# Performance work log

Hardware: AMD Instinct MI355X
Metric: run time of the kernel (lower is better)

## Reference

```python
import jax, jax.numpy as jnp
import numpy as np

EMB = 1024
CTX = 32
F_IN, R, F_OUT = 1024, 16, 1024
N_EXP = 16
H1 = 2048   # expert / gating hidden
H2 = 512    # expert output width
B = 8


def _init(key, shape, fan_in):
    return jax.random.normal(key, shape, dtype=jnp.float32) / np.sqrt(fan_in)


def setup_inputs() -> dict:
    key = jax.random.key(0)
    ks = jax.random.split(key, 14)
    return {
        "s": jax.random.normal(ks[0], (B, EMB), dtype=jnp.float32),
        # gating: Linear(EMB,2048) -> ReLU -> Linear(2048,N_EXP) -> Softmax
        "Wg1": _init(ks[1], (EMB, H1), EMB),
        "bg1": jnp.zeros((H1,), jnp.float32),
        "Wg2": _init(ks[2], (H1, N_EXP), H1),
        "bg2": jnp.zeros((N_EXP,), jnp.float32),
        # experts (stacked): Linear(EMB+CTX,2048) -> ReLU -> Linear(2048,512)
        "W1": _init(ks[3], (N_EXP, EMB + CTX, H1), EMB + CTX),
        "b1": jnp.zeros((N_EXP, H1), jnp.float32),
        "W2": _init(ks[4], (N_EXP, H1, H2), H1),
        "b2": jnp.zeros((N_EXP, H2), jnp.float32),
        # decoders
        "WA": _init(ks[5], (H2, F_IN * R), H2),
        "bA": jnp.zeros((F_IN * R,), jnp.float32),
        "WB": _init(ks[6], (H2, R * F_OUT), H2),
        "bB": jnp.zeros((R * F_OUT,), jnp.float32),
    }


def reference(s, Wg1, bg1, Wg2, bg2, W1, b1, W2, b2, WA, bA, WB, bB):
    # gating weights over experts: [B, E]
    weights = jax.nn.softmax(jax.nn.relu(s @ Wg1 + bg1) @ Wg2 + bg2, axis=-1)

    # Expert layer-1. Input is concat([s, one_hot(c)]); since the context part
    # is a one-hot, its contribution is just a row of the context block of W1.
    W1s = W1[:, :EMB, :]              # [E, EMB, H1]
    W1c = W1[:, EMB:, :]              # [E, CTX, H1]
    base = jnp.einsum('bi,eih->ebh', s, W1s) + b1[:, None, :]   # [E, B, H1]
    # h[c,e,b,:] = relu(base[e,b,:] + W1c[e,c,:])
    h = jax.nn.relu(base[None] + jnp.transpose(W1c, (1, 0, 2))[:, :, None, :])  # [C,E,B,H1]

    # Expert layer-2: [C, E, B, H2]
    eo = jnp.einsum('cebh,ehd->cebd', h, W2) + b2[None, :, None, :]

    # softmax-weighted mixture over experts: [C, B, H2]
    z = jnp.einsum('be,cebd->cbd', weights, eo)

    A = (z @ WA + bA).reshape(CTX, B, F_IN, R)
    Bm = (z @ WB + bB).reshape(CTX, B, R, F_OUT)
    return A, Bm
```

## Files before the change

### kernel.cpp

```cpp
#include <hip/hip_runtime.h>
#include <hip/hip_bf16.h>

#define EMB 1024
#define CTX 32
#define NEXP 16
#define H1 2048
#define H2 512
#define NBIG 16384

typedef __attribute__((ext_vector_type(8))) short short8;
typedef __attribute__((ext_vector_type(4))) float floatx4;
typedef __attribute__((ext_vector_type(2))) unsigned uint2v;
typedef const __attribute__((address_space(1))) void* gas_t;
typedef __attribute__((address_space(3))) void* las_t;

__device__ __forceinline__ void gl16(const unsigned short* g, unsigned short* l) {
  __builtin_amdgcn_global_load_lds((gas_t)(const void*)g, (las_t)(void*)l, 16, 0, 0);
}

__device__ inline unsigned short bf_bits(float x) {
  unsigned u = __builtin_bit_cast(unsigned, x);
  u += 0x7fffu + ((u >> 16) & 1u);
  return (unsigned short)(u >> 16);
}
__device__ inline unsigned pk_bf16(float a, float b) {
  return (unsigned)bf_bits(a) | ((unsigned)bf_bits(b) << 16);
}

__global__ void __launch_bounds__(512) k_fusedA(const float* __restrict__ s,
                                                const float* __restrict__ Wg1,
                                                const float* __restrict__ bg1,
                                                const float* __restrict__ W1,
                                                const float* __restrict__ b1,
                                                const float* __restrict__ W2,
                                                float* __restrict__ g1,
                                                float* __restrict__ base,
                                                unsigned short* __restrict__ W2t) {
  __shared__ __align__(16) char smem[34816];
  int bid = blockIdx.x;
  int t = threadIdx.x;

  if (bid < 256) {
    float* sl = (float*)smem;
    int ht = bid & 15;
    int e = bid >> 4;
#pragma unroll
    for (int i = 0; i < 4; ++i) {
      int idx = (t + i * 512) * 4;
      *(float4*)&sl[idx] = *(const float4*)&s[idx];
    }
    __syncthreads();
    int hp = t & 63;
    int kk = t >> 6;
    int h = ht * 128 + hp * 2;
    const float* wp = W1 + (size_t)e * 1056 * H1 + h;
    float a0[8], a1[8];
#pragma unroll
    for (int b = 0; b < 8; ++b) { a0[b] = 0.f; a1[b] = 0.f; }
    int k0 = kk * 128;
#pragma unroll 4
    for (int k = k0; k < k0 + 128; ++k) {
      float2 w = *(const float2*)(wp + (size_t)k * H1);
#pragma unroll
      for (int b = 0; b < 8; ++b) {
        float sv = sl[b * EMB + k];
        a0[b] += sv * w.x;
        a1[b] += sv * w.y;
      }
    }
    __syncthreads();
    float(*red)[64][17] = (float(*)[64][17])smem;
#pragma unroll
    for (int b = 0; b < 8; ++b) {
      red[kk][hp][b * 2] = a0[b];
      red[kk][hp][b * 2 + 1] = a1[b];
    }
    __syncthreads();
    if (t < 64) {
      int hh = ht * 128 + t * 2;
#pragma unroll
      for (int b = 0; b < 8; ++b) {
        float v0 = 0.f, v1 = 0.f;
#pragma unroll
        for (int q = 0; q < 8; ++q) {
          v0 += red[q][t][b * 2];
          v1 += red[q][t][b * 2 + 1];
        }
        float2 bv = *(const float2*)&b1[e * H1 + hh];
        float2 o;
        o.x = v0 + bv.x;
        o.y = v1 + bv.y;
        *(float2*)&base[(size_t)(e * 8 + b) * H1 + hh] = o;
      }
    }
  } else if (bid < 4352) {
    float(*tl)[65] = (float(*)[65])smem;
    int pid = bid - 256;
    int nt = pid & 7, kb = (pid >> 3) & 31, e = pid >> 8;
    const float* S = W2 + (size_t)e * H1 * H2 + (size_t)kb * 64 * H2 + nt * 64;
    int r = t >> 4, c4 = (t & 15) * 4;
#pragma unroll
    for (int i = 0; i < 2; ++i) {
      int row = r + i * 32;
      float4 v = *(const float4*)&S[(size_t)row * H2 + c4];
      *(float4*)&tl[row][c4] = v;
    }
    __syncthreads();
    int nl = t >> 3;
    int cp = t & 7;
    int key = nl & 7;
    unsigned short* D = W2t + (size_t)e * 1048576 +
                        ((size_t)kb * 512 + nt * 64 + nl) * 64;
    int k0 = (cp ^ key) * 8;
    union { short8 v; unsigned u[4]; } p;
#pragma unroll
    for (int q = 0; q < 4; ++q)
      p.u[q] = pk_bf16(tl[k0 + 2 * q][nl], tl[k0 + 2 * q + 1][nl]);
    *(short8*)&D[cp * 8] = p.v;
  } else {
    float(*red1)[16][8] = (float(*)[16][8])smem;
    int gid = bid - 4352;
    int c = t & 15, kk = t >> 4;
    int h = gid * 16 + c;
    float acc[8];
#pragma unroll
    for (int b = 0; b < 8; ++b) acc[b] = 0.f;
    int k0 = kk * 32;
    for (int k = k0; k < k0 + 32; ++k) {
      float w = Wg1[(size_t)k * H1 + h];
#pragma unroll
      for (int b = 0; b < 8; ++b) acc[b] += s[b * EMB + k] * w;
    }
#pragma unroll
    for (int b = 0; b < 8; ++b) red1[kk][c][b] = acc[b];
    __syncthreads();
    if (t < 128) {
      int cc = t >> 3, b = t & 7;
      float v = 0.f;
#pragma unroll
      for (int q = 0; q < 32; ++q) v += red1[q][cc][b];
      int hh = gid * 16 + cc;
      v += bg1[hh];
      g1[b * H1 + hh] = fmaxf(v, 0.f);
    }
  }
}

__global__ void __launch_bounds__(512) k_fusedB(const float* __restrict__ base,
                                                const float* __restrict__ W1,
                                                const unsigned short* __restrict__ W2t,
                                                const float* __restrict__ g1,
                                                const float* __restrict__ Wg2,
                                                const float* __restrict__ bg2,
                                                float* __restrict__ eo2,
                                                float* __restrict__ logits) {
  __shared__ __align__(16) char smemB[40960];
  int bid = blockIdx.x;
  int t = threadIdx.x;

  if (bid < 256) {
    unsigned short* As = (unsigned short*)smemB;
    unsigned short* Bs = (unsigned short*)(smemB + 8192);
    int id = bid;
    int mt = id >> 6, rem = id & 63;
    int e = rem >> 2, nt = (rem >> 1) & 1, ks = rem & 1;
    int lane = t & 63, w = t >> 6;
    int wm = w >> 2, wn = w & 3;
    int fr = lane & 15, quad = lane >> 4, key = fr & 7;

    int am = t >> 3;
    int ak = (t & 7) * 8;
    const float* bp = base + ((size_t)e * 8 + (am & 7)) * H1;
    const float* cp = W1 + ((size_t)e * 1056 + EMB + mt * 8 + (am >> 3)) * H1;
    unsigned short* adst = &As[am * 64 + (((t & 7) ^ (am & 7)) * 8)];
    const unsigned short* wBe = W2t + (size_t)e * 1048576 + (size_t)nt * 16384;

    floatx4 zero4 = {0.f, 0.f, 0.f, 0.f};
    floatx4 acc[2][4];
#pragma unroll
    for (int i = 0; i < 2; ++i)
#pragma unroll
      for (int j = 0; j < 4; ++j) acc[i][j] = zero4;

    for (int i = 0; i < 16; ++i) {
      int kb = ks * 16 + i;
      __syncthreads();
      const unsigned short* bsrc = wBe + (size_t)kb * 32768 + t * 8;
      gl16(bsrc, &Bs[t * 8]);
      gl16(bsrc + 4096, &Bs[t * 8 + 4096]);
      gl16(bsrc + 8192, &Bs[t * 8 + 8192]);
      gl16(bsrc + 12288, &Bs[t * 8 + 12288]);
      int k0 = kb * 64 + ak;
      float4 x0 = *(const float4*)&bp[k0];
      float4 x1 = *(const float4*)&bp[k0 + 4];
      float4 y0 = *(const float4*)&cp[k0];
      float4 y1 = *(const float4*)&cp[k0 + 4];
      union { short8 v; unsigned u[4]; } pq;
      pq.u[0] = pk_bf16(fmaxf(x0.x + y0.x, 0.f), fmaxf(x0.y + y0.y, 0.f));
      pq.u[1] = pk_bf16(fmaxf(x0.z + y0.z, 0.f), fmaxf(x0.w + y0.w, 0.f));
      pq.u[2] = pk_bf16(fmaxf(x1.x + y1.x, 0.f), fmaxf(x1.y + y1.y, 0.f));
      pq.u[3] = pk_bf16(fmaxf(x1.z + y1.z, 0.f), fmaxf(x1.w + y1.w, 0.f));
      *(short8*)adst = pq.v;
      __syncthreads();
#pragma unroll
      for (int ks2 = 0; ks2 < 2; ++ks2) {
        int cof = ((ks2 * 4 + quad) ^ key) * 8;
        short8 a0 = *(const short8*)&As[(wm * 32 + fr) * 64 + cof];
        short8 a1 = *(const short8*)&As[(wm * 32 + 16 + fr) * 64 + cof];
#pragma unroll
        for (int nj = 0; nj < 4; ++nj) {
          short8 bf = *(const short8*)&Bs[(wn * 64 + nj * 16 + fr) * 64 + cof];
          acc[0][nj] = __builtin_amdgcn_mfma_f32_16x16x32_bf16(a0, bf, acc[0][nj], 0, 0, 0);
          acc[1][nj] = __builtin_amdgcn_mfma_f32_16x16x32_bf16(a1, bf, acc[1][nj], 0, 0, 0);
        }
      }
    }
    float* op = eo2 + (size_t)ks * 2097152;
    int d0 = nt * 256 + wn * 64 + fr;
#pragma unroll
    for (int nj = 0; nj < 4; ++nj) {
      int d = d0 + nj * 16;
#pragma unroll
      for (int rt = 0; rt < 2; ++rt) {
#pragma unroll
        for (int i2 = 0; i2 < 4; ++i2) {
          int gm = mt * 64 + wm * 32 + rt * 16 + quad * 4 + i2;
          op[(((size_t)(gm >> 3) * NEXP + e) * 8 + (gm & 7)) * H2 + d] = acc[rt][nj][i2];
        }
      }
    }
  } else {
    float(*red)[8] = (float(*)[8])smemB;
    int e = bid - 256;
    int k0 = t * 4;
    float wv[4];
#pragma unroll
    for (int j = 0; j < 4; ++j) wv[j] = Wg2[(size_t)(k0 + j) * NEXP + e];
    float acc[8];
#pragma unroll
    for (int b = 0; b < 8; ++b) {
      float4 ga = *(const float4*)&g1[b * H1 + k0];
      acc[b] = ga.x * wv[0] + ga.y * wv[1] + ga.z * wv[2] + ga.w * wv[3];
    }
#pragma unroll
    for (int b = 0; b < 8; ++b) red[t][b] = acc[b];
    __syncthreads();
    for (int off = 256; off > 0; off >>= 1) {
      if (t < off) {
#pragma unroll
        for (int b = 0; b < 8; ++b) red[t][b] += red[t + off][b];
      }
      __syncthreads();
    }
    if (t < 8) logits[t * NEXP + e] = red[0][t] + bg2[e];
  }
}

__global__ void __launch_bounds__(256) k_mix(const float* __restrict__ eo2,
                                             const float* __restrict__ logits,
                                             const float* __restrict__ b2,
                                             unsigned short* __restrict__ z_t) {
  int c = blockIdx.x, by = blockIdx.y, t = threadIdx.x;
  int b = t >> 5;
  int x = t & 31;
  int dc = by * 16 + (x >> 1);
  int part = x & 1;
  int d0 = dc * 8 + part * 4;
  int m = c * 8 + b;
  float lg[16];
  float mx = -1e30f;
#pragma unroll
  for (int e = 0; e < 16; ++e) {
    lg[e] = logits[b * NEXP + e];
    mx = fmaxf(mx, lg[e]);
  }
  float sum = 0.f;
#pragma unroll
  for (int e = 0; e < 16; ++e) {
    lg[e] = __expf(lg[e] - mx);
    sum += lg[e];
  }
  float inv = 1.f / sum;
  float o[4];
#pragma unroll
  for (int j = 0; j < 4; ++j) o[j] = 0.f;
#pragma unroll
  for (int e = 0; e < 16; ++e) {
    float wl = lg[e] * inv;
    const float* p = &eo2[(((size_t)c * NEXP + e) * 8 + b) * H2 + d0];
    float4 x0 = *(const float4*)p;
    float4 y0 = *(const float4*)(p + 2097152);
    float4 v0 = *(const float4*)&b2[e * H2 + d0];
    o[0] += wl * (x0.x + y0.x + v0.x);
    o[1] += wl * (x0.y + y0.y + v0.y);
    o[2] += wl * (x0.z + y0.z + v0.z);
    o[3] += wl * (x0.w + y0.w + v0.w);
  }
  uint2v p;
  p.x = pk_bf16(o[0], o[1]);
  p.y = pk_bf16(o[2], o[3]);
  int kb = dc >> 3;
  int cpx = (dc & 7) ^ (b & 7);
  *(uint2v*)&z_t[((size_t)kb * 256 + m) * 64 + cpx * 8 + part * 4] = p;
}

__global__ void __launch_bounds__(512) k_lora2(const unsigned short* __restrict__ z_t,
                                               const float* __restrict__ WA,
                                               const float* __restrict__ WB,
                                               const float* __restrict__ bA,
                                               const float* __restrict__ bB,
                                               float* __restrict__ out) {
  __shared__ __align__(16) unsigned short As[16384];
  __shared__ __align__(16) unsigned short Bs[8192];
  int nt = blockIdx.x;
  int t = threadIdx.x, lane = t & 63, w = t >> 6;
  int wm = w >> 1, wn = w & 1;
  int fr = lane & 15, quad = lane >> 4, key = fr & 7;
  int ms = nt >> 7;
  const float* Wsrc = ms ? WB : WA;
  int col0 = (nt & 127) * 128;
  int bn = t & 127, kg = t >> 7;
  const float* bw = Wsrc + col0 + bn;
  unsigned short* bd0 = &Bs[bn * 64 + (((kg * 2) ^ (bn & 7)) * 8)];
  unsigned short* bd1 = &Bs[bn * 64 + (((kg * 2 + 1) ^ (bn & 7)) * 8)];

  floatx4 zero4 = {0.f, 0.f, 0.f, 0.f};
  floatx4 acc[4][4];
#pragma unroll
  for (int i = 0; i < 4; ++i)
#pragma unroll
    for (int j = 0; j < 4; ++j) acc[i][j] = zero4;

  for (int kb = 0; kb < 8; ++kb) {
    __syncthreads();
    const unsigned short* asrc = z_t + (size_t)kb * 16384 + t * 8;
    gl16(asrc, &As[t * 8]);
    gl16(asrc + 4096, &As[t * 8 + 4096]);
    gl16(asrc + 8192, &As[t * 8 + 8192]);
    gl16(asrc + 12288, &As[t * 8 + 12288]);
    const float* bk = bw + (size_t)(kb * 64 + kg * 16) * NBIG;
    float v[16];
#pragma unroll
    for (int kr = 0; kr < 16; ++kr) v[kr] = bk[(size_t)kr * NBIG];
    union { short8 s; unsigned u[4]; } q0, q1;
#pragma unroll
    for (int q = 0; q < 4; ++q) {
      q0.u[q] = pk_bf16(v[2 * q], v[2 * q + 1]);
      q1.u[q] = pk_bf16(v[8 + 2 * q], v[9 + 2 * q]);
    }
    *(short8*)bd0 = q0.s;
    *(short8*)bd1 = q1.s;
    __syncthreads();
#pragma unroll
    for (int ks2 = 0; ks2 < 2; ++ks2) {
      int cof = ((ks2 * 4 + quad) ^ key) * 8;
      short8 bf0 = *(const short8*)&Bs[(wn * 64 + fr) * 64 + cof];
      short8 bf1 = *(const short8*)&Bs[(wn * 64 + 16 + fr) * 64 + cof];
      short8 bf2 = *(const short8*)&Bs[(wn * 64 + 32 + fr) * 64 + cof];
      short8 bf3 = *(const short8*)&Bs[(wn * 64 + 48 + fr) * 64 + cof];
#pragma unroll
      for (int rt = 0; rt < 4; ++rt) {
        short8 af = *(const short8*)&As[(wm * 64 + rt * 16 + fr) * 64 + cof];
        acc[rt][0] = __builtin_amdgcn_mfma_f32_16x16x32_bf16(af, bf0, acc[rt][0], 0, 0, 0);
        acc[rt][1] = __builtin_amdgcn_mfma_f32_16x16x32_bf16(af, bf1, acc[rt][1], 0, 0, 0);
        acc[rt][2] = __builtin_amdgcn_mfma_f32_16x16x32_bf16(af, bf2, acc[rt][2], 0, 0, 0);
        acc[rt][3] = __builtin_amdgcn_mfma_f32_16x16x32_bf16(af, bf3, acc[rt][3], 0, 0, 0);
      }
    }
  }
  const float* bias = ms ? bB : bA;
  float* obase = out + (size_t)ms * 4194304;
#pragma unroll
  for (int nj = 0; nj < 4; ++nj) {
    int nn = col0 + wn * 64 + nj * 16 + fr;
    float bv = bias[nn];
#pragma unroll
    for (int rt = 0; rt < 4; ++rt) {
#pragma unroll
      for (int i2 = 0; i2 < 4; ++i2) {
        int m = wm * 64 + rt * 16 + quad * 4 + i2;
        obase[(size_t)m * NBIG + nn] = acc[rt][nj][i2] + bv;
      }
    }
  }
}

extern "C" void kernel_launch(void* const* d_in, const int* in_sizes, int n_in,
                              void* d_out, int out_size, void* d_ws, size_t ws_size,
                              hipStream_t stream) {
  const float* s = (const float*)d_in[0];
  const float* Wg1 = (const float*)d_in[1];
  const float* bg1 = (const float*)d_in[2];
  const float* Wg2 = (const float*)d_in[3];
  const float* bg2 = (const float*)d_in[4];
  const float* W1 = (const float*)d_in[5];
  const float* b1 = (const float*)d_in[6];
  const float* W2 = (const float*)d_in[7];
  const float* b2 = (const float*)d_in[8];
  const float* WA = (const float*)d_in[9];
  const float* bA = (const float*)d_in[10];
  const float* WB = (const float*)d_in[11];
  const float* bB = (const float*)d_in[12];
  float* out = (float*)d_out;

  char* ws = (char*)d_ws;
  float* g1 = (float*)(ws);
  float* logits = (float*)(ws + 65536);
  float* base = (float*)(ws + 131072);
  float* eo2 = (float*)(ws + 1179648);
  unsigned short* z_t = (unsigned short*)(ws + 17956864);
  unsigned short* W2t = (unsigned short*)(ws + 18219008);

  k_fusedA<<<4480, 512, 0, stream>>>(s, Wg1, bg1, W1, b1, W2, g1, base, W2t);
  k_fusedB<<<272, 512, 0, stream>>>(base, W1, W2t, g1, Wg2, bg2, eo2, logits);
  k_mix<<<dim3(32, 4), 256, 0, stream>>>(eo2, logits, b2, z_t);
  k_lora2<<<256, 512, 0, stream>>>(z_t, WA, WB, bA, bB, out);
}
```

Measured before the change: 371.3 us.

## Merge gating layer-1 into expert GEMV path with wider per-thread tiles

```diff
diff --git a/kernel.cpp b/kernel.cpp
--- a/kernel.cpp
+++ b/kernel.cpp
@@ -27,7 +27,7 @@
   return (unsigned)bf_bits(a) | ((unsigned)bf_bits(b) << 16);
 }
 
-__global__ void __launch_bounds__(512) k_fusedA(const float* __restrict__ s,
+__global__ void __launch_bounds__(256) k_fusedA(const float* __restrict__ s,
                                                 const float* __restrict__ Wg1,
                                                 const float* __restrict__ bg1,
                                                 const float* __restrict__ W1,
@@ -36,112 +36,99 @@
                                                 float* __restrict__ g1,
                                                 float* __restrict__ base,
                                                 unsigned short* __restrict__ W2t) {
-  __shared__ __align__(16) char smem[34816];
+  __shared__ __align__(16) char smem[36864];
   int bid = blockIdx.x;
   int t = threadIdx.x;
 
-  if (bid < 256) {
-    float* sl = (float*)smem;
-    int ht = bid & 15;
-    int e = bid >> 4;
-#pragma unroll
-    for (int i = 0; i < 4; ++i) {
-      int idx = (t + i * 512) * 4;
-      *(float4*)&sl[idx] = *(const float4*)&s[idx];
-    }
-    __syncthreads();
-    int hp = t & 63;
-    int kk = t >> 6;
-    int h = ht * 128 + hp * 2;
-    const float* wp = W1 + (size_t)e * 1056 * H1 + h;
-    float a0[8], a1[8];
-#pragma unroll
-    for (int b = 0; b < 8; ++b) { a0[b] = 0.f; a1[b] = 0.f; }
+  if (bid < 272) {
+    int wi = bid >> 4, tile = bid & 15;
+    int h0 = tile * 128;
+    float* st = (float*)smem;
+    {
+      int b = t >> 5, kc = (t & 31) * 32;
+      const float* sp = s + (size_t)b * EMB + kc;
+#pragma unroll
+      for (int j = 0; j < 32; j += 4) {
+        float4 v = *(const float4*)&sp[j];
+        st[(kc + j) * 8 + b] = v.x;
+        st[(kc + j + 1) * 8 + b] = v.y;
+        st[(kc + j + 2) * 8 + b] = v.z;
+        st[(kc + j + 3) * 8 + b] = v.w;
+      }
+    }
+    __syncthreads();
+    int hp = t & 31, kk = t >> 5;
+    const float* wp = (wi < 16 ? W1 + (size_t)wi * 1056 * H1 : Wg1) + h0 + hp * 4;
+    floatx4 a[8];
+#pragma unroll
+    for (int b = 0; b < 8; ++b) a[b] = (floatx4){0.f, 0.f, 0.f, 0.f};
     int k0 = kk * 128;
 #pragma unroll 4
     for (int k = k0; k < k0 + 128; ++k) {
-      float2 w = *(const float2*)(wp + (size_t)k * H1);
-#pragma unroll
-      for (int b = 0; b < 8; ++b) {
-        float sv = sl[b * EMB + k];
-        a0[b] += sv * w.x;
-        a1[b] += sv * w.y;
-      }
-    }
-    __syncthreads();
-    float(*red)[64][17] = (float(*)[64][17])smem;
-#pragma unroll
-    for (int b = 0; b < 8; ++b) {
-      red[kk][hp][b * 2] = a0[b];
-      red[kk][hp][b * 2 + 1] = a1[b];
-    }
-    __syncthreads();
-    if (t < 64) {
-      int hh = ht * 128 + t * 2;
-#pragma unroll
-      for (int b = 0; b < 8; ++b) {
-        float v0 = 0.f, v1 = 0.f;
-#pragma unroll
-        for (int q = 0; q < 8; ++q) {
-          v0 += red[q][t][b * 2];
-          v1 += red[q][t][b * 2 + 1];
-        }
-        float2 bv = *(const float2*)&b1[e * H1 + hh];
-        float2 o;
-        o.x = v0 + bv.x;
-        o.y = v1 + bv.y;
-        *(float2*)&base[(size_t)(e * 8 + b) * H1 + hh] = o;
-      }
-    }
-  } else if (bid < 4352) {
+      floatx4 w = *(const floatx4*)(wp + (size_t)k * H1);
+      float4 s0 = *(const float4*)&st[k * 8];
+      float4 s1 = *(const float4*)&st[k * 8 + 4];
+      a[0] += s0.x * w;
+      a[1] += s0.y * w;
+      a[2] += s0.z * w;
+      a[3] += s0.w * w;
+      a[4] += s1.x * w;
+      a[5] += s1.y * w;
+      a[6] += s1.z * w;
+      a[7] += s1.w * w;
+    }
+    __syncthreads();
+    float* red = (float*)smem;
+#pragma unroll
+    for (int b = 0; b < 8; ++b)
+      *(floatx4*)&red[(kk * 32 + hp) * 36 + b * 4] = a[b];
+    __syncthreads();
+    {
+      int b = t >> 5, hp2 = t & 31;
+      floatx4 v = (floatx4){0.f, 0.f, 0.f, 0.f};
+#pragma unroll
+      for (int q = 0; q < 8; ++q)
+        v += *(const floatx4*)&red[(q * 32 + hp2) * 36 + b * 4];
+      int h = h0 + hp2 * 4;
+      if (wi < 16) {
+        floatx4 bv = *(const floatx4*)&b1[wi * H1 + h];
+        v += bv;
+        *(floatx4*)&base[(size_t)(wi * 8 + b) * H1 + h] = v;
+      } else {
+        floatx4 bv = *(const floatx4*)&bg1[h];
+        v += bv;
+        floatx4 z = (floatx4){0.f, 0.f, 0.f, 0.f};
+        v = __builtin_elementwise_max(v, z);
+        *(floatx4*)&g1[(size_t)b * H1 + h] = v;
+      }
+    }
+  } else {
     float(*tl)[65] = (float(*)[65])smem;
-    int pid = bid - 256;
+    int pid = bid - 272;
     int nt = pid & 7, kb = (pid >> 3) & 31, e = pid >> 8;
     const float* S = W2 + (size_t)e * H1 * H2 + (size_t)kb * 64 * H2 + nt * 64;
     int r = t >> 4, c4 = (t & 15) * 4;
 #pragma unroll
-    for (int i = 0; i < 2; ++i) {
-      int row = r + i * 32;
+    for (int i = 0; i < 4; ++i) {
+      int row = r + i * 16;
       float4 v = *(const float4*)&S[(size_t)row * H2 + c4];
       *(float4*)&tl[row][c4] = v;
     }
     __syncthreads();
-    int nl = t >> 3;
-    int cp = t & 7;
+    int nl = t >> 2;
+    int cb = (t & 3) * 2;
     int key = nl & 7;
     unsigned short* D = W2t + (size_t)e * 1048576 +
                         ((size_t)kb * 512 + nt * 64 + nl) * 64;
-    int k0 = (cp ^ key) * 8;
-    union { short8 v; unsigned u[4]; } p;
-#pragma unroll
-    for (int q = 0; q < 4; ++q)
-      p.u[q] = pk_bf16(tl[k0 + 2 * q][nl], tl[k0 + 2 * q + 1][nl]);
-    *(short8*)&D[cp * 8] = p.v;
-  } else {
-    float(*red1)[16][8] = (float(*)[16][8])smem;
-    int gid = bid - 4352;
-    int c = t & 15, kk = t >> 4;
-    int h = gid * 16 + c;
-    float acc[8];
-#pragma unroll
-    for (int b = 0; b < 8; ++b) acc[b] = 0.f;
-    int k0 = kk * 32;
-    for (int k = k0; k < k0 + 32; ++k) {
-      float w = Wg1[(size_t)k * H1 + h];
-#pragma unroll
-      for (int b = 0; b < 8; ++b) acc[b] += s[b * EMB + k] * w;
-    }
-#pragma unroll
-    for (int b = 0; b < 8; ++b) red1[kk][c][b] = acc[b];
-    __syncthreads();
-    if (t < 128) {
-      int cc = t >> 3, b = t & 7;
-      float v = 0.f;
-#pragma unroll
-      for (int q = 0; q < 32; ++q) v += red1[q][cc][b];
-      int hh = gid * 16 + cc;
-      v += bg1[hh];
-      g1[b * H1 + hh] = fmaxf(v, 0.f);
+#pragma unroll
+    for (int j = 0; j < 2; ++j) {
+      int cp = cb + j;
+      int k0 = (cp ^ key) * 8;
+      union { short8 v; unsigned u[4]; } p;
+#pragma unroll
+      for (int q = 0; q < 4; ++q)
+        p.u[q] = pk_bf16(tl[k0 + 2 * q][nl], tl[k0 + 2 * q + 1][nl]);
+      *(short8*)&D[cp * 8] = p.v;
     }
   }
 }
@@ -411,7 +398,7 @@
   unsigned short* z_t = (unsigned short*)(ws + 17956864);
   unsigned short* W2t = (unsigned short*)(ws + 18219008);
 
-  k_fusedA<<<4480, 512, 0, stream>>>(s, Wg1, bg1, W1, b1, W2, g1, base, W2t);
+  k_fusedA<<<4368, 256, 0, stream>>>(s, Wg1, bg1, W1, b1, W2, g1, base, W2t);
   k_fusedB<<<272, 512, 0, stream>>>(base, W1, W2t, g1, Wg2, bg2, eo2, logits);
   k_mix<<<dim3(32, 4), 256, 0, stream>>>(eo2, logits, b2, z_t);
   k_lora2<<<256, 512, 0, stream>>>(z_t, WA, WB, bA, bB, out);
```

After: 370.5 us. About the same (-0.2%).
